# Kernel optimization log

Hardware: AMD Instinct MI355X
Metric: run time of the kernel (lower is better)

The kernel has to match this reference:

```python
import jax, jax.numpy as jnp
import numpy as np

FIR = (1.0, 3.0, 3.0, 1.0)

def _fir_kernel():
    k = jnp.array(FIR, dtype=jnp.float32)
    k = jnp.outer(k, k)
    return k / jnp.sum(k)  # gain = 1

def setup_inputs() -> dict:
    key = jax.random.key(0)
    k1, k2, k3 = jax.random.split(key, 3)
    N, C, H, W = 8, 512, 64, 64
    return {
        "hidden_states": jax.random.normal(k1, (N, C, H, W), jnp.float32),
        "weight": jax.random.normal(k2, (512, 512, 3, 3), jnp.float32) * 0.02,
        "bias": jax.random.normal(k3, (512,), jnp.float32) * 0.01,
    }

def reference(hidden_states, weight, bias):
    # FirDownsample2D forward, use_conv=True, factor=2, fir_kernel=(1,3,3,1).
    # pad_value = kH - factor + (convW - 1) = 4 - 2 + 2 = 4 -> pad = (2, 2)
    k = _fir_kernel()  # [4,4], normalized
    C = hidden_states.shape[1]
    # upfirdn2d_native with up=1, down=1: pad spatially then per-channel
    # cross-correlation with the FLIPPED kernel (== true convolution).
    kf = jnp.flip(k, (0, 1)).astype(hidden_states.dtype)
    kf = jnp.broadcast_to(kf[None, None], (C, 1, 4, 4))  # depthwise [C,1,4,4]
    y = jax.lax.conv_general_dilated(
        hidden_states, kf, window_strides=(1, 1), padding=[(2, 2), (2, 2)],
        dimension_numbers=("NCHW", "OIHW", "NCHW"), feature_group_count=C)
    # y: [N, C, H+1, W+1]; fused 3x3 conv, stride=factor=2, no padding.
    out = jax.lax.conv_general_dilated(
        y, weight, window_strides=(2, 2), padding="VALID",
        dimension_numbers=("NCHW", "OIHW", "NCHW"))  # [N, Cout, H//2, W//2]
    return out + bias[None, :, None, None]
```

## Files before the change

### kernel.cpp

```cpp
#include <hip/hip_runtime.h>
#include <stdint.h>

#define CI 512
#define CO 512
#define HI 64
#define WI 64
#define HY 65
#define NB 8

typedef __bf16 bf16x8 __attribute__((ext_vector_type(8)));
typedef float f32x4 __attribute__((ext_vector_type(4)));

__device__ __forceinline__ unsigned short f2bf(float f) {
  unsigned int u = __float_as_uint(f);
  return (unsigned short)((u + 0x7fffu + ((u >> 16) & 1u)) >> 16);
}

__device__ __forceinline__ void async16(void* lds, const void* g) {
  __builtin_amdgcn_global_load_lds(
      (const __attribute__((address_space(1))) uint32_t*)g,
      (__attribute__((address_space(3))) uint32_t*)lds, 16, 0, 0);
}

#define CT 32
#define RT 13

__global__ __launch_bounds__(256) void fir_kernel(const float* __restrict__ x,
                                                  unsigned short* __restrict__ yt) {
  __shared__ float raw[CT][WI + 1];
  __shared__ float hrow[4][HY][CT];

  const int tid = threadIdx.x;
  const int bid = blockIdx.x;
  const int n = bid / 80;
  const int rem = bid % 80;
  const int c0 = (rem / 5) * CT;
  const int r0 = (rem % 5) * RT;

  const float* xb = x + ((size_t)n * CI + c0) * (HI * WI);

  const int lc = tid >> 3;
  const int lq = tid & 7;
  const int c = tid & (CT - 1);
  const int sb = tid >> 5;

  auto stage = [&](int hr) {
    __syncthreads();
    if ((unsigned)hr < (unsigned)HI) {
      const float* rowp = xb + ((size_t)lc * HI + hr) * WI;
      float4 a = *(const float4*)&rowp[lq * 4];
      float4 b = *(const float4*)&rowp[(lq + 8) * 4];
      raw[lc][lq * 4 + 0] = a.x; raw[lc][lq * 4 + 1] = a.y;
      raw[lc][lq * 4 + 2] = a.z; raw[lc][lq * 4 + 3] = a.w;
      raw[lc][(lq + 8) * 4 + 0] = b.x; raw[lc][(lq + 8) * 4 + 1] = b.y;
      raw[lc][(lq + 8) * 4 + 2] = b.z; raw[lc][(lq + 8) * 4 + 3] = b.w;
    }
    __syncthreads();
    const int slot = hr & 3;
    if ((unsigned)hr < (unsigned)HI) {
#pragma unroll
      for (int k = 0; k < 9; k++) {
        const int s = sb + (k << 3);
        if (s < HY) {
          float v = 0.f;
          if (s >= 2) v += raw[c][s - 2];
          if (s >= 1) v += 3.f * raw[c][s - 1];
          if (s <= 63) v += 3.f * raw[c][s];
          if (s <= 62) v += raw[c][s + 1];
          hrow[slot][s][c] = v;
        }
      }
    } else {
#pragma unroll
      for (int k = 0; k < 9; k++) {
        const int s = sb + (k << 3);
        if (s < HY) hrow[slot][s][c] = 0.f;
      }
    }
  };

  stage(r0 - 2);
  stage(r0 - 1);
  stage(r0);

  for (int i = 0; i < RT; i++) {
    const int r = r0 + i;
    stage(r + 1);
    __syncthreads();
    const int q0 = (r - 2) & 3, q1 = (r - 1) & 3, q2 = r & 3, q3 = (r + 1) & 3;
    unsigned short* yo = yt + (((size_t)n * HY + r) * HY) * CI + c0 + c;
#pragma unroll
    for (int k = 0; k < 9; k++) {
      const int s = sb + (k << 3);
      if (s < HY) {
        const float y = (hrow[q0][s][c] + 3.f * hrow[q1][s][c] +
                         3.f * hrow[q2][s][c] + hrow[q3][s][c]) * (1.f / 64.f);
        yo[(size_t)s * CI] = f2bf(y);
      }
    }
  }
}

__global__ __launch_bounds__(256) void wt_kernel(const float* __restrict__ w,
                                                 unsigned short* __restrict__ wtb) {
  const int gid = blockIdx.x * 256 + threadIdx.x;
  const int ci = gid & (CI - 1);
  const int co = gid >> 9;
  const float* src = w + ((size_t)co * CI + ci) * 9;
#pragma unroll
  for (int t = 0; t < 9; t++) {
    wtb[((size_t)t * CO + co) * CI + ci] = f2bf(src[t]);
  }
}

__global__ __launch_bounds__(256, 2) void conv_kernel(
    const unsigned short* __restrict__ wtb,
    const unsigned short* __restrict__ yt,
    const float* __restrict__ bias,
    float* __restrict__ out) {
  __shared__ unsigned short Alds[2][64 * 64];
  __shared__ unsigned short Blds[2][128 * 64];

  const int tid = threadIdx.x;
  const int wgid = ((blockIdx.x & 7) << 6) | (blockIdx.x >> 3);
  const int co_t = (wgid & 7) << 6;
  const int m0 = (wgid >> 3) << 7;
  const int n = m0 >> 10;
  const int w = tid >> 6, l = tid & 63;

  size_t aoff[2];
#pragma unroll
  for (int i = 0; i < 2; i++) {
    const int cch = i * 256 + w * 64 + l;
    const int row = cch >> 3, s = cch & 7;
    aoff[i] = (size_t)(co_t + row) * CI + ((s ^ (row & 7)) << 3);
  }
  size_t boff[4];
#pragma unroll
  for (int i = 0; i < 4; i++) {
    const int cch = i * 256 + w * 64 + l;
    const int p = cch >> 3, s = cch & 7;
    const int pos = m0 + p;
    const int ho = (pos & 1023) >> 5, wo = pos & 31;
    boff[i] = (((size_t)n * HY + 2 * ho) * HY + 2 * wo) * CI + ((s ^ (p & 7)) << 3);
  }

  auto stage = [&](int b, int ks) {
    const int tap = ks >> 3;
    const int ci0 = (ks & 7) << 6;
    const int kh = tap / 3, kw = tap - kh * 3;
    const size_t ka = (size_t)tap * (CO * CI) + ci0;
    const size_t kb = (size_t)(kh * HY + kw) * CI + ci0;
    unsigned short* Ab = &Alds[b][0];
    unsigned short* Bb = &Blds[b][0];
#pragma unroll
    for (int i = 0; i < 2; i++)
      async16(Ab + (size_t)(i * 256 + w * 64 + l) * 8, wtb + ka + aoff[i]);
#pragma unroll
    for (int i = 0; i < 4; i++)
      async16(Bb + (size_t)(i * 256 + w * 64 + l) * 8, yt + kb + boff[i]);
  };

  const int wco = (w >> 1) << 5;
  const int wpos = (w & 1) << 6;
  const int ll = l & 15, kg = l >> 4;
  const int a7 = ll & 7;

  int aidx[2][2], bidx[4][2];
#pragma unroll
  for (int m = 0; m < 2; m++)
#pragma unroll
    for (int kk = 0; kk < 2; kk++)
      aidx[m][kk] = (wco + m * 16 + ll) * 64 + ((((kk << 2) | kg) ^ a7) << 3);
#pragma unroll
  for (int nf = 0; nf < 4; nf++)
#pragma unroll
    for (int kk = 0; kk < 2; kk++)
      bidx[nf][kk] = (wpos + nf * 16 + ll) * 64 + ((((kk << 2) | kg) ^ a7) << 3);

  f32x4 acc[2][4] = {};

  stage(0, 0);
  __syncthreads();

  int cur = 0;
  for (int ks = 0; ks < 72; ks++) {
    if (ks < 71) stage(cur ^ 1, ks + 1);
    const unsigned short* Ac = &Alds[cur][0];
    const unsigned short* Bc = &Blds[cur][0];
#pragma unroll
    for (int kk = 0; kk < 2; kk++) {
      const bf16x8 a0 = *(const bf16x8*)(Ac + aidx[0][kk]);
      const bf16x8 a1 = *(const bf16x8*)(Ac + aidx[1][kk]);
      const bf16x8 b0 = *(const bf16x8*)(Bc + bidx[0][kk]);
      const bf16x8 b1 = *(const bf16x8*)(Bc + bidx[1][kk]);
      const bf16x8 b2 = *(const bf16x8*)(Bc + bidx[2][kk]);
      const bf16x8 b3 = *(const bf16x8*)(Bc + bidx[3][kk]);
      acc[0][0] = __builtin_amdgcn_mfma_f32_16x16x32_bf16(a0, b0, acc[0][0], 0, 0, 0);
      acc[0][1] = __builtin_amdgcn_mfma_f32_16x16x32_bf16(a0, b1, acc[0][1], 0, 0, 0);
      acc[0][2] = __builtin_amdgcn_mfma_f32_16x16x32_bf16(a0, b2, acc[0][2], 0, 0, 0);
      acc[0][3] = __builtin_amdgcn_mfma_f32_16x16x32_bf16(a0, b3, acc[0][3], 0, 0, 0);
      acc[1][0] = __builtin_amdgcn_mfma_f32_16x16x32_bf16(a1, b0, acc[1][0], 0, 0, 0);
      acc[1][1] = __builtin_amdgcn_mfma_f32_16x16x32_bf16(a1, b1, acc[1][1], 0, 0, 0);
      acc[1][2] = __builtin_amdgcn_mfma_f32_16x16x32_bf16(a1, b2, acc[1][2], 0, 0, 0);
      acc[1][3] = __builtin_amdgcn_mfma_f32_16x16x32_bf16(a1, b3, acc[1][3], 0, 0, 0);
    }
    __syncthreads();
    cur ^= 1;
  }

#pragma unroll
  for (int i = 0; i < 2; i++) {
#pragma unroll
    for (int r = 0; r < 4; r++) {
      const int co = co_t + wco + i * 16 + kg * 4 + r;
      const float bv = bias[co];
#pragma unroll
      for (int j = 0; j < 4; j++) {
        const int pos = m0 + wpos + j * 16 + ll;
        const int ho = (pos & 1023) >> 5;
        const int wo = pos & 31;
        out[(((size_t)n * CO + co) * 32 + ho) * 32 + wo] = acc[i][j][r] + bv;
      }
    }
  }
}

extern "C" void kernel_launch(void* const* d_in, const int* in_sizes, int n_in,
                              void* d_out, int out_size, void* d_ws, size_t ws_size,
                              hipStream_t stream) {
  const float* x = (const float*)d_in[0];
  const float* w = (const float*)d_in[1];
  const float* bias = (const float*)d_in[2];
  float* out = (float*)d_out;

  unsigned short* yt = (unsigned short*)d_ws;
  unsigned short* wtb = yt + (size_t)NB * HY * HY * CI;

  fir_kernel<<<NB * (CI / CT) * 5, 256, 0, stream>>>(x, yt);
  wt_kernel<<<(CO * CI) / 256, 256, 0, stream>>>(w, wtb);
  conv_kernel<<<512, 256, 0, stream>>>(wtb, yt, bias, out);
}
```

Baseline: 95.73 us.

## Enlarge conv tiles to 128x256, split K in two with atomic accumulation, triple-buffer

The conv GEMM now runs 512-thread blocks on 128 output-channel by 256 position tiles, with each wave holding a 64x64 accumulator. The reduction dimension is split in half across two blocks, and their partial sums are combined with float atomicAdd into an output that a new init kernel first fills with bias. LDS staging moves from double to triple buffering with explicit vmcnt waits and raw barriers, and MFMA sections are given raised wave priority. The intent is more data reuse per LDS load and deeper load/compute overlap. The cost is an extra kernel, atomic traffic on the output, more LDS use, and non-deterministic summation order.

```diff
diff --git a/kernel.cpp b/kernel.cpp
--- a/kernel.cpp
+++ b/kernel.cpp
@@ -113,114 +113,146 @@
   }
 }
 
-__global__ __launch_bounds__(256, 2) void conv_kernel(
+__global__ __launch_bounds__(256) void init_kernel(const float* __restrict__ bias,
+                                                   float* __restrict__ out) {
+  const int gid = blockIdx.x * 256 + threadIdx.x;
+  const float bv = bias[(gid >> 8) & 511];
+  float4 v = {bv, bv, bv, bv};
+  *(float4*)(out + (size_t)gid * 4) = v;
+}
+
+__global__ __launch_bounds__(512, 2) void conv_kernel(
     const unsigned short* __restrict__ wtb,
     const unsigned short* __restrict__ yt,
-    const float* __restrict__ bias,
     float* __restrict__ out) {
-  __shared__ unsigned short Alds[2][64 * 64];
-  __shared__ unsigned short Blds[2][128 * 64];
+  __shared__ unsigned short Alds[3][128 * 64];
+  __shared__ unsigned short Blds[3][256 * 64];
 
   const int tid = threadIdx.x;
-  const int wgid = ((blockIdx.x & 7) << 6) | (blockIdx.x >> 3);
-  const int co_t = (wgid & 7) << 6;
-  const int m0 = (wgid >> 3) << 7;
+  const int xcd = blockIdx.x & 7;
+  const int j = blockIdx.x >> 3;
+  const int pos_tile = xcd * 4 + (j >> 3);
+  const int variant = j & 7;
+  const int co_t = (variant >> 1) << 7;
+  const int split = variant & 1;
+  const int ks0 = split * 36;
+  const int m0 = pos_tile << 8;
   const int n = m0 >> 10;
-  const int w = tid >> 6, l = tid & 63;
-
-  size_t aoff[2];
+
+  uint32_t aoff[2];
 #pragma unroll
   for (int i = 0; i < 2; i++) {
-    const int cch = i * 256 + w * 64 + l;
-    const int row = cch >> 3, s = cch & 7;
-    aoff[i] = (size_t)(co_t + row) * CI + ((s ^ (row & 7)) << 3);
-  }
-  size_t boff[4];
+    const int ch = tid + i * 512;
+    const int row = ch >> 3, s = ch & 7;
+    aoff[i] = (uint32_t)((co_t + row) * CI + ((s ^ (row & 7)) << 3));
+  }
+  uint32_t boff[4];
 #pragma unroll
   for (int i = 0; i < 4; i++) {
-    const int cch = i * 256 + w * 64 + l;
-    const int p = cch >> 3, s = cch & 7;
+    const int ch = tid + i * 512;
+    const int p = ch >> 3, s = ch & 7;
     const int pos = m0 + p;
     const int ho = (pos & 1023) >> 5, wo = pos & 31;
-    boff[i] = (((size_t)n * HY + 2 * ho) * HY + 2 * wo) * CI + ((s ^ (p & 7)) << 3);
-  }
-
-  auto stage = [&](int b, int ks) {
-    const int tap = ks >> 3;
-    const int ci0 = (ks & 7) << 6;
+    boff[i] = (uint32_t)(((n * HY + 2 * ho) * HY + 2 * wo) * CI + ((s ^ (p & 7)) << 3));
+  }
+
+  auto stg = [&](unsigned short* Ab, unsigned short* Bb, int gks) {
+    const int tap = gks >> 3;
+    const int ci0 = (gks & 7) << 6;
     const int kh = tap / 3, kw = tap - kh * 3;
-    const size_t ka = (size_t)tap * (CO * CI) + ci0;
-    const size_t kb = (size_t)(kh * HY + kw) * CI + ci0;
-    unsigned short* Ab = &Alds[b][0];
-    unsigned short* Bb = &Blds[b][0];
+    const unsigned short* wsrc = wtb + (size_t)tap * (CO * CI) + ci0;
+    const unsigned short* ysrc = yt + (size_t)(kh * HY + kw) * CI + ci0;
 #pragma unroll
     for (int i = 0; i < 2; i++)
-      async16(Ab + (size_t)(i * 256 + w * 64 + l) * 8, wtb + ka + aoff[i]);
+      async16(Ab + (size_t)(tid + i * 512) * 8, wsrc + aoff[i]);
 #pragma unroll
     for (int i = 0; i < 4; i++)
-      async16(Bb + (size_t)(i * 256 + w * 64 + l) * 8, yt + kb + boff[i]);
+      async16(Bb + (size_t)(tid + i * 512) * 8, ysrc + boff[i]);
   };
 
-  const int wco = (w >> 1) << 5;
-  const int wpos = (w & 1) << 6;
+  const int wv = tid >> 6;
+  const int wcoW = (wv >> 2) << 6;
+  const int wposW = (wv & 3) << 6;
+  const int l = tid & 63;
   const int ll = l & 15, kg = l >> 4;
   const int a7 = ll & 7;
 
-  int aidx[2][2], bidx[4][2];
-#pragma unroll
-  for (int m = 0; m < 2; m++)
+  int aidx[4][2], bidx[4][2];
+#pragma unroll
+  for (int m = 0; m < 4; m++)
 #pragma unroll
     for (int kk = 0; kk < 2; kk++)
-      aidx[m][kk] = (wco + m * 16 + ll) * 64 + ((((kk << 2) | kg) ^ a7) << 3);
+      aidx[m][kk] = (wcoW + m * 16 + ll) * 64 + ((((kk << 2) | kg) ^ a7) << 3);
 #pragma unroll
   for (int nf = 0; nf < 4; nf++)
 #pragma unroll
     for (int kk = 0; kk < 2; kk++)
-      bidx[nf][kk] = (wpos + nf * 16 + ll) * 64 + ((((kk << 2) | kg) ^ a7) << 3);
-
-  f32x4 acc[2][4] = {};
-
-  stage(0, 0);
-  __syncthreads();
-
-  int cur = 0;
-  for (int ks = 0; ks < 72; ks++) {
-    if (ks < 71) stage(cur ^ 1, ks + 1);
-    const unsigned short* Ac = &Alds[cur][0];
-    const unsigned short* Bc = &Blds[cur][0];
-#pragma unroll
-    for (int kk = 0; kk < 2; kk++) {
-      const bf16x8 a0 = *(const bf16x8*)(Ac + aidx[0][kk]);
-      const bf16x8 a1 = *(const bf16x8*)(Ac + aidx[1][kk]);
-      const bf16x8 b0 = *(const bf16x8*)(Bc + bidx[0][kk]);
-      const bf16x8 b1 = *(const bf16x8*)(Bc + bidx[1][kk]);
-      const bf16x8 b2 = *(const bf16x8*)(Bc + bidx[2][kk]);
-      const bf16x8 b3 = *(const bf16x8*)(Bc + bidx[3][kk]);
-      acc[0][0] = __builtin_amdgcn_mfma_f32_16x16x32_bf16(a0, b0, acc[0][0], 0, 0, 0);
-      acc[0][1] = __builtin_amdgcn_mfma_f32_16x16x32_bf16(a0, b1, acc[0][1], 0, 0, 0);
-      acc[0][2] = __builtin_amdgcn_mfma_f32_16x16x32_bf16(a0, b2, acc[0][2], 0, 0, 0);
-      acc[0][3] = __builtin_amdgcn_mfma_f32_16x16x32_bf16(a0, b3, acc[0][3], 0, 0, 0);
-      acc[1][0] = __builtin_amdgcn_mfma_f32_16x16x32_bf16(a1, b0, acc[1][0], 0, 0, 0);
-      acc[1][1] = __builtin_amdgcn_mfma_f32_16x16x32_bf16(a1, b1, acc[1][1], 0, 0, 0);
-      acc[1][2] = __builtin_amdgcn_mfma_f32_16x16x32_bf16(a1, b2, acc[1][2], 0, 0, 0);
-      acc[1][3] = __builtin_amdgcn_mfma_f32_16x16x32_bf16(a1, b3, acc[1][3], 0, 0, 0);
-    }
-    __syncthreads();
-    cur ^= 1;
-  }
-
-#pragma unroll
-  for (int i = 0; i < 2; i++) {
+      bidx[nf][kk] = (wposW + nf * 16 + ll) * 64 + ((((kk << 2) | kg) ^ a7) << 3);
+
+  f32x4 acc[4][4] = {};
+
+  stg(&Alds[0][0], &Blds[0][0], ks0);
+  stg(&Alds[1][0], &Blds[1][0], ks0 + 1);
+  asm volatile("s_waitcnt vmcnt(6)" ::: "memory");
+  __builtin_amdgcn_s_barrier();
+
+#define COMPUTE(CUR)                                                        \
+  {                                                                         \
+    const unsigned short* Ac = &Alds[CUR][0];                               \
+    const unsigned short* Bc = &Blds[CUR][0];                               \
+    _Pragma("unroll") for (int kk = 0; kk < 2; kk++) {                      \
+      const bf16x8 a0 = *(const bf16x8*)(Ac + aidx[0][kk]);                 \
+      const bf16x8 a1 = *(const bf16x8*)(Ac + aidx[1][kk]);                 \
+      const bf16x8 a2 = *(const bf16x8*)(Ac + aidx[2][kk]);                 \
+      const bf16x8 a3 = *(const bf16x8*)(Ac + aidx[3][kk]);                 \
+      const bf16x8 b0 = *(const bf16x8*)(Bc + bidx[0][kk]);                 \
+      const bf16x8 b1 = *(const bf16x8*)(Bc + bidx[1][kk]);                 \
+      const bf16x8 b2 = *(const bf16x8*)(Bc + bidx[2][kk]);                 \
+      const bf16x8 b3 = *(const bf16x8*)(Bc + bidx[3][kk]);                 \
+      __builtin_amdgcn_s_setprio(1);                                        \
+      _Pragma("unroll") for (int m = 0; m < 4; m++) {                       \
+        const bf16x8 am = (m == 0) ? a0 : (m == 1) ? a1 : (m == 2) ? a2 : a3; \
+        acc[m][0] = __builtin_amdgcn_mfma_f32_16x16x32_bf16(am, b0, acc[m][0], 0, 0, 0); \
+        acc[m][1] = __builtin_amdgcn_mfma_f32_16x16x32_bf16(am, b1, acc[m][1], 0, 0, 0); \
+        acc[m][2] = __builtin_amdgcn_mfma_f32_16x16x32_bf16(am, b2, acc[m][2], 0, 0, 0); \
+        acc[m][3] = __builtin_amdgcn_mfma_f32_16x16x32_bf16(am, b3, acc[m][3], 0, 0, 0); \
+      }                                                                     \
+      __builtin_amdgcn_s_setprio(0);                                        \
+    }                                                                       \
+  }
+
+#define ITER(CUR, NXT, KSL)                                                 \
+  {                                                                         \
+    const int ksl = (KSL);                                                  \
+    if (ksl + 2 < 36) stg(&Alds[NXT][0], &Blds[NXT][0], ks0 + ksl + 2);     \
+    COMPUTE(CUR);                                                           \
+    if (ksl < 34) {                                                         \
+      asm volatile("s_waitcnt vmcnt(6)" ::: "memory");                      \
+      __builtin_amdgcn_s_barrier();                                         \
+    } else if (ksl == 34) {                                                 \
+      asm volatile("s_waitcnt vmcnt(0)" ::: "memory");                      \
+      __builtin_amdgcn_s_barrier();                                         \
+    }                                                                       \
+  }
+
+  for (int kb = 0; kb < 36; kb += 3) {
+    ITER(0, 2, kb);
+    ITER(1, 0, kb + 1);
+    ITER(2, 1, kb + 2);
+  }
+#undef ITER
+#undef COMPUTE
+
+#pragma unroll
+  for (int m = 0; m < 4; m++) {
 #pragma unroll
     for (int r = 0; r < 4; r++) {
-      const int co = co_t + wco + i * 16 + kg * 4 + r;
-      const float bv = bias[co];
-#pragma unroll
-      for (int j = 0; j < 4; j++) {
-        const int pos = m0 + wpos + j * 16 + ll;
-        const int ho = (pos & 1023) >> 5;
-        const int wo = pos & 31;
-        out[(((size_t)n * CO + co) * 32 + ho) * 32 + wo] = acc[i][j][r] + bv;
+      const int co = co_t + wcoW + m * 16 + kg * 4 + r;
+      float* orow = out + ((size_t)n * CO + co) * 1024;
+#pragma unroll
+      for (int nf = 0; nf < 4; nf++) {
+        const int pos = m0 + wposW + nf * 16 + ll;
+        atomicAdd(orow + (pos & 1023), acc[m][nf][r]);
       }
     }
   }
@@ -239,5 +271,6 @@
 
   fir_kernel<<<NB * (CI / CT) * 5, 256, 0, stream>>>(x, yt);
   wt_kernel<<<(CO * CI) / 256, 256, 0, stream>>>(w, wtb);
-  conv_kernel<<<512, 256, 0, stream>>>(wtb, yt, bias, out);
-}
+  init_kernel<<<4096, 256, 0, stream>>>(bias, out);
+  conv_kernel<<<256, 512, 0, stream>>>(wtb, yt, out);
+}
```

Measured after the change: 103.5 us. 1.08x slower.

## Split conv K dimension in two with atomic accumulation and bias-init kernel

Applied to the files above, without the earlier changes.

The conv GEMM's 72-step K loop is split into two halves run by separate workgroups, doubling the grid from 512 to 1024 blocks so a 256-CU device is better occupied. Partial sums are combined with float atomicAdd into an output that a new init kernel pre-fills with bias. The blocks are also remapped so that each XCD keeps the same position tiles, aiming for better L2 reuse, and the occupancy hint rises to 3 blocks per CU. The cost is an extra kernel launch, a full write of the output before accumulation, atomic traffic on the output, and summation order that is no longer deterministic.

```diff
diff --git a/kernel.cpp b/kernel.cpp
--- a/kernel.cpp
+++ b/kernel.cpp
@@ -113,18 +113,30 @@
   }
 }
 
-__global__ __launch_bounds__(256, 2) void conv_kernel(
+__global__ __launch_bounds__(256) void init_kernel(const float* __restrict__ bias,
+                                                   float* __restrict__ out) {
+  const int gid = blockIdx.x * 256 + threadIdx.x;
+  const float bv = bias[(gid >> 8) & 511];
+  float4 v = {bv, bv, bv, bv};
+  *(float4*)(out + (size_t)gid * 4) = v;
+}
+
+__global__ __launch_bounds__(256, 3) void conv_kernel(
     const unsigned short* __restrict__ wtb,
     const unsigned short* __restrict__ yt,
-    const float* __restrict__ bias,
     float* __restrict__ out) {
   __shared__ unsigned short Alds[2][64 * 64];
   __shared__ unsigned short Blds[2][128 * 64];
 
   const int tid = threadIdx.x;
-  const int wgid = ((blockIdx.x & 7) << 6) | (blockIdx.x >> 3);
-  const int co_t = (wgid & 7) << 6;
-  const int m0 = (wgid >> 3) << 7;
+  const int xcd = blockIdx.x & 7;
+  const int j = blockIdx.x >> 3;
+  const int pos_tile = xcd * 8 + (j >> 4);
+  const int variant = j & 15;
+  const int co_t = (variant >> 1) << 6;
+  const int split = variant & 1;
+  const int ks0 = split * 36;
+  const int m0 = pos_tile << 7;
   const int n = m0 >> 10;
   const int w = tid >> 6, l = tid & 63;
 
@@ -180,12 +192,12 @@
 
   f32x4 acc[2][4] = {};
 
-  stage(0, 0);
+  stage(0, ks0);
   __syncthreads();
 
   int cur = 0;
-  for (int ks = 0; ks < 72; ks++) {
-    if (ks < 71) stage(cur ^ 1, ks + 1);
+  for (int t = 0; t < 36; t++) {
+    if (t < 35) stage(cur ^ 1, ks0 + t + 1);
     const unsigned short* Ac = &Alds[cur][0];
     const unsigned short* Bc = &Blds[cur][0];
 #pragma unroll
@@ -214,13 +226,11 @@
 #pragma unroll
     for (int r = 0; r < 4; r++) {
       const int co = co_t + wco + i * 16 + kg * 4 + r;
-      const float bv = bias[co];
-#pragma unroll
-      for (int j = 0; j < 4; j++) {
-        const int pos = m0 + wpos + j * 16 + ll;
-        const int ho = (pos & 1023) >> 5;
-        const int wo = pos & 31;
-        out[(((size_t)n * CO + co) * 32 + ho) * 32 + wo] = acc[i][j][r] + bv;
+      float* orow = out + ((size_t)n * CO + co) * 1024;
+#pragma unroll
+      for (int jf = 0; jf < 4; jf++) {
+        const int pos = m0 + wpos + jf * 16 + ll;
+        atomicAdd(orow + (pos & 1023), acc[i][jf][r]);
       }
     }
   }
@@ -239,5 +249,6 @@
 
   fir_kernel<<<NB * (CI / CT) * 5, 256, 0, stream>>>(x, yt);
   wt_kernel<<<(CO * CI) / 256, 256, 0, stream>>>(w, wtb);
-  conv_kernel<<<512, 256, 0, stream>>>(wtb, yt, bias, out);
-}
+  init_kernel<<<4096, 256, 0, stream>>>(bias, out);
+  conv_kernel<<<1024, 256, 0, stream>>>(wtb, yt, out);
+}
```

After: 119.5 us. 24.8% more time.
